# Optimization experiments

Hardware: AMD Instinct MI355X
Metric: run time of the kernel (lower is better)

## Reference

```python
import jax, jax.numpy as jnp
import numpy as np

B, T, S = 32, 64, 400
EMB = ENC = DEC = ATT = 512
POOL = 2
VOCAB = 32000
L = 1
NEG = 1e12  # INF constant from the torch source


def setup_inputs():
    key = jax.random.key(0)
    ks = jax.random.split(key, 16)
    def p(i, shape, s=0.05):
        return jax.random.normal(ks[i], shape, jnp.float32) * s
    return {
        "trg_seq_embedded": jax.random.normal(ks[0], (B, T, EMB), jnp.float32),
        "enc_states": jax.random.normal(ks[1], (L, B, ENC), jnp.float32),
        "encoder_outputs": jax.random.normal(ks[2], (B, S, ENC), jnp.float32),
        "W_trans": p(3, (DEC, ENC)), "b_trans": jnp.zeros((DEC,), jnp.float32),
        "W_ih": p(4, (3 * DEC, EMB + ENC)), "W_hh": p(5, (3 * DEC, DEC)),
        "b_ih": jnp.zeros((3 * DEC,), jnp.float32), "b_hh": jnp.zeros((3 * DEC,), jnp.float32),
        "W_pre": p(6, (ATT, ENC)), "b_pre": jnp.zeros((ATT,), jnp.float32),
        "W_q": p(7, (ATT, DEC)), "W_cov": p(8, (ATT, 1)), "v_att": p(9, (ATT,)),
        "W_ro": p(10, (DEC, ENC + DEC + EMB)), "b_ro": jnp.zeros((DEC,), jnp.float32),
        "W_logit": p(11, (VOCAB, DEC // POOL)), "b_logit": jnp.zeros((VOCAB,), jnp.float32),
        "ext_src_seq": jax.random.randint(ks[12], (B, S), 0, VOCAB + 50),
        "encoder_mask": jnp.zeros((B, S), jnp.bool_),  # True = padding position
    }


def _gru_cell(x, h, W_ih, W_hh, b_ih, b_hh):
    # torch.nn.GRUCell semantics, gate order r, z, n
    gi = x @ W_ih.T + b_ih
    gh = h @ W_hh.T + b_hh
    ir, iz, inn = jnp.split(gi, 3, axis=1)
    hr, hz, hn = jnp.split(gh, 3, axis=1)
    r = jax.nn.sigmoid(ir + hr)
    z = jax.nn.sigmoid(iz + hz)
    n = jnp.tanh(inn + r * hn)
    return (1.0 - z) * n + z * h


def _forward(trg, enc_states, memories, params, ext_src_seq, mask):
    (W_trans, b_trans, W_ih, W_hh, b_ih, b_hh, W_pre, b_pre, W_q, W_cov,
     v_att, W_ro, b_ro, W_logit, b_logit) = params
    # num_oov computed eagerly from the (constant) extended source ids
    num_oov = max(int(jnp.max(ext_src_seq)) - VOCAB + 1, 0)
    b_idx = jnp.arange(B)[:, None]
    precompute = memories @ W_pre.T + b_pre          # [B,S,ATT], computed once
    h0 = enc_states @ W_trans.T + b_trans            # [L,B,DEC] init_rnn_hidden
    c0 = jnp.zeros((B, ENC), trg.dtype)              # pre_context
    cov0 = jnp.zeros((B, S), trg.dtype)              # coverage

    def step(carry, emb):
        h, ctx, cov = carry
        x = jnp.concatenate([emb, ctx], axis=1)      # input_feed
        h_new = _gru_cell(x, h[0], W_ih, W_hh, b_ih, b_hh)  # single-layer StackedGRU
        out = h_new
        # ConcatAttention with coverage term
        target = out @ W_q.T                                    # [B,ATT]
        cov_term = cov[:, :, None] * W_cov[:, 0][None, None, :]  # [B,S,ATT]
        energy = jnp.tanh(precompute + target[:, None, :] + cov_term) @ v_att  # [B,S]
        energy = jnp.where(mask, -NEG, energy)
        score = jax.nn.softmax(energy, axis=1)
        context = jnp.einsum('bs,bse->be', score, memories)
        # readout -> maxout -> logits
        readout = jnp.concatenate([emb, out, context], axis=1) @ W_ro.T + b_ro
        mo = readout.reshape(B, DEC // POOL, POOL).max(axis=-1)
        logit = mo @ W_logit.T + b_logit
        # pointer: scatter_max of energy into extended vocab
        ext_logit = jnp.concatenate([logit, jnp.zeros((B, num_oov), logit.dtype)], axis=1)
        scat = jnp.full((B, VOCAB + num_oov), -NEG, logit.dtype)
        scat = scat.at[b_idx, ext_src_seq].max(energy)
        scat = jnp.where(scat == -NEG, 0.0, scat)
        logit = ext_logit + scat
        logit = jnp.where(logit == 0.0, -NEG, logit)
        return (h_new[None], context, cov + score), (logit, score, cov)

    _, (logits, attn, cov_hist) = jax.lax.scan(step, (h0, c0, cov0), jnp.swapaxes(trg, 0, 1))
    return jnp.swapaxes(logits, 0, 1), attn, cov_hist


def reference(trg_seq_embedded, enc_states, encoder_outputs, W_trans, b_trans, W_ih, W_hh, b_ih, b_hh, W_pre, b_pre, W_q, W_cov, v_att, W_ro, b_ro, W_logit, b_logit, ext_src_seq, encoder_mask):
    params = (W_trans, b_trans, W_ih, W_hh, b_ih, b_hh, W_pre, b_pre, W_q, W_cov,
              v_att, W_ro, b_ro, W_logit, b_logit)
    return _forward(trg_seq_embedded, enc_states, encoder_outputs, params, ext_src_seq, encoder_mask)
```

## Files before the change

kernel.cpp:

```cpp
#include <hip/hip_runtime.h>

#define Bz 32
#define Tz 64
#define Sz 400
#define Dz 512
#define G3 1536
#define VOC 32000
#define NEGC 1e12f
#define SB 50
#define JB 8

typedef __attribute__((ext_vector_type(8))) short short8;
typedef __attribute__((ext_vector_type(8))) _Float16 h8;
typedef __attribute__((ext_vector_type(4))) float f32x4;
typedef __attribute__((ext_vector_type(4))) unsigned u32x4;
typedef __attribute__((ext_vector_type(2))) _Float16 half2_t;

__device__ __forceinline__ float sigm(float x){ return 1.f/(1.f+__expf(-x)); }
__device__ __forceinline__ float tanhfast(float x){ float e=__expf(2.f*x); return 1.f - 2.f/(e+1.f); }
__device__ __forceinline__ unsigned short f2bf(float f){
  unsigned int u = __float_as_uint(f);
  u = (u + 0x7FFFu + ((u>>16)&1u)) >> 16;
  return (unsigned short)u;
}
__device__ __forceinline__ unsigned f2bf2(float a, float b){
  return (unsigned)f2bf(a) | ((unsigned)f2bf(b) << 16);
}
__device__ __forceinline__ half2_t bch2(unsigned u){ return __builtin_bit_cast(half2_t, u); }
__device__ __forceinline__ unsigned packh2(float a, float b){
  unsigned short ua = __builtin_bit_cast(unsigned short, (_Float16)a);
  unsigned short ub = __builtin_bit_cast(unsigned short, (_Float16)b);
  return (unsigned)ua | ((unsigned)ub << 16);
}

__device__ __forceinline__ float aload_f(const float* p){
  unsigned v = __hip_atomic_load((unsigned*)p, __ATOMIC_RELAXED, __HIP_MEMORY_SCOPE_AGENT);
  return __uint_as_float(v);
}
__device__ __forceinline__ unsigned long long aload_u64(const void* p){
  return __hip_atomic_load((const unsigned long long*)p, __ATOMIC_RELAXED, __HIP_MEMORY_SCOPE_AGENT);
}
__device__ __forceinline__ void astore_f(float* p, float v){
  __hip_atomic_store((unsigned*)p, __float_as_uint(v), __ATOMIC_RELAXED, __HIP_MEMORY_SCOPE_AGENT);
}
__device__ __forceinline__ void astore_u32(unsigned* p, unsigned v){
  __hip_atomic_store(p, v, __ATOMIC_RELAXED, __HIP_MEMORY_SCOPE_AGENT);
}

#if defined(__has_builtin)
#if __has_builtin(__builtin_amdgcn_fdot2)
#define HAVE_FDOT2 1
#endif
#endif
#ifdef HAVE_FDOT2
__device__ __forceinline__ float FDOT(half2_t a, half2_t b, float c){
  return __builtin_amdgcn_fdot2(a, b, c, false);
}
#else
__device__ __forceinline__ float FDOT(half2_t a, half2_t b, float c){
  return c + (float)a[0]*(float)b[0] + (float)a[1]*(float)b[1];
}
#endif

__global__ __launch_bounds__(128) void repack_emb(const float* __restrict__ emb,
    unsigned short* __restrict__ emb2, unsigned short* __restrict__ rinb){
  int tb = blockIdx.x; int t = tb >> 5, b = tb & 31;
  int e4 = threadIdx.x;
  float4 v = *(const float4*)&emb[((size_t)b*Tz + t)*Dz + e4*4];
  unsigned* e2 = (unsigned*)&emb2[(size_t)tb*Dz + e4*4];
  e2[0] = packh2(v.x, v.y);
  e2[1] = packh2(v.z, v.w);
  unsigned* rb = (unsigned*)&rinb[(size_t)tb*G3 + e4*4];
  rb[0] = f2bf2(v.x, v.y);
  rb[1] = f2bf2(v.z, v.w);
}

__global__ __launch_bounds__(256) void wgj_pack(const float* __restrict__ W_ih,
    const float* __restrict__ W_hh, unsigned* __restrict__ Wg){
  int idx = blockIdx.x*256 + threadIdx.x;
  int i = idx & 31, oct = (idx>>5)&7;
  int ks = idx >> 8;
  int s = ks % 6, k = ks / 6;
  int e0 = (oct*32 + i)*2;
  float w0, w1;
  if (s < 3){
    const float* base = W_ih + ((size_t)(s*512 + k))*1024 + 512;
    w0 = base[e0]; w1 = base[e0+1];
  } else {
    const float* base = W_hh + ((size_t)((s-3)*512 + k))*512;
    w0 = base[e0]; w1 = base[e0+1];
  }
  Wg[idx] = packh2(w0, w1);
}

__global__ __launch_bounds__(256) void wq2_pack(const float* __restrict__ W_q,
    unsigned* __restrict__ Wq2){
  int idx = blockIdx.x*256 + threadIdx.x;
  int jj = idx & 511;
  int i  = (idx>>9) & 31;
  int js = idx >> 14;
  int k0 = js*64 + 2*i;
  Wq2[idx] = packh2(W_q[(size_t)jj*512 + k0], W_q[(size_t)jj*512 + k0 + 1]);
}

__global__ __launch_bounds__(256) void cast_f16(const float* __restrict__ in,
    unsigned short* __restrict__ out, int n){
  for (int i = blockIdx.x*256 + threadIdx.x; i < n; i += gridDim.x*256)
    out[i] = __builtin_bit_cast(unsigned short, (_Float16)in[i]);
}

__global__ __launch_bounds__(256) void cast_f16_str(const float* __restrict__ in, int ldi,
    unsigned short* __restrict__ out, int cols, int n){
  for (int i = blockIdx.x*256 + threadIdx.x; i < n; i += gridDim.x*256){
    int r = i / cols, c = i - r*cols;
    out[i] = __builtin_bit_cast(unsigned short, (_Float16)in[(size_t)r*ldi + c]);
  }
}

__global__ __launch_bounds__(256) void cast_bf(const float* __restrict__ in,
    unsigned short* __restrict__ out, int n){
  for (int i = blockIdx.x*256 + threadIdx.x; i < n; i += gridDim.x*256)
    out[i] = f2bf(in[i]);
}

__global__ __launch_bounds__(256) void zero_u32(unsigned* __restrict__ p, int n){
  int i = blockIdx.x*256 + threadIdx.x;
  if (i < n) p[i] = 0u;
}

__global__ __launch_bounds__(256) void gemm_f32(const float* __restrict__ A, int lda,
    const float* __restrict__ Bm, int ldb, const float* __restrict__ bias,
    float* __restrict__ C, int ldc, int M, int N, int K){
  __shared__ __align__(16) float As[16][68];
  __shared__ __align__(16) float Bs[16][68];
  int tid = threadIdx.x;
  int m0 = blockIdx.x * 64, n0 = blockIdx.y * 64;
  int tx = tid & 15, ty = tid >> 4;
  float acc[4][4] = {};
  int lr = tid >> 2;
  int lk = (tid & 3) << 2;
  for (int k0 = 0; k0 < K; k0 += 16){
    int m = m0 + lr;
    float4 va = (m < M) ? *(const float4*)&A[(size_t)m*lda + k0 + lk] : make_float4(0,0,0,0);
    int n = n0 + lr;
    float4 vb = (n < N) ? *(const float4*)&Bm[(size_t)n*ldb + k0 + lk] : make_float4(0,0,0,0);
    As[lk+0][lr]=va.x; As[lk+1][lr]=va.y; As[lk+2][lr]=va.z; As[lk+3][lr]=va.w;
    Bs[lk+0][lr]=vb.x; Bs[lk+1][lr]=vb.y; Bs[lk+2][lr]=vb.z; Bs[lk+3][lr]=vb.w;
    __syncthreads();
    #pragma unroll
    for (int kk = 0; kk < 16; kk++){
      float4 a = *(const float4*)&As[kk][ty*4];
      float4 b = *(const float4*)&Bs[kk][tx*4];
      float av[4] = {a.x,a.y,a.z,a.w};
      float bv[4] = {b.x,b.y,b.z,b.w};
      #pragma unroll
      for (int i = 0; i < 4; i++)
        #pragma unroll
        for (int j = 0; j < 4; j++)
          acc[i][j] += av[i]*bv[j];
    }
    __syncthreads();
  }
  #pragma unroll
  for (int i = 0; i < 4; i++){
    int m = m0 + ty*4 + i;
    if (m >= M) continue;
    #pragma unroll
    for (int j = 0; j < 4; j++){
      int n = n0 + tx*4 + j;
      if (n < N) C[(size_t)m*ldc + n] = acc[i][j] + bias[n];
    }
  }
}

__global__ __launch_bounds__(256) void mfma_bf16(const unsigned short* __restrict__ A, int lda,
    const unsigned short* __restrict__ Bm, int ldb, const float* __restrict__ bias,
    float* __restrict__ out, int N, int K, int mode, int Vext){
  __shared__ __align__(16) unsigned short As[128][40];
  __shared__ __align__(16) unsigned short Bs[128][40];
  int tid = threadIdx.x;
  int m0 = blockIdx.x * 128, n0 = blockIdx.y * 128;
  int wid = tid >> 6, lane = tid & 63;
  int wm = (wid >> 1) * 64, wn = (wid & 1) * 64;
  f32x4 acc[4][4];
  #pragma unroll
  for (int r = 0; r < 4; r++)
    #pragma unroll
    for (int c = 0; c < 4; c++) acc[r][c] = (f32x4){0.f,0.f,0.f,0.f};
  int lr = tid >> 1;
  int lk = (tid & 1) * 16;
  int frow = lane & 15, kg = (lane >> 4) * 8;
  for (int k0 = 0; k0 < K; k0 += 32){
    *(uint4*)&As[lr][lk]     = *(const uint4*)&A[(size_t)(m0+lr)*lda + k0 + lk];
    *(uint4*)&As[lr][lk+8]   = *(const uint4*)&A[(size_t)(m0+lr)*lda + k0 + lk + 8];
    *(uint4*)&Bs[lr][lk]     = *(const uint4*)&Bm[(size_t)(n0+lr)*ldb + k0 + lk];
    *(uint4*)&Bs[lr][lk+8]   = *(const uint4*)&Bm[(size_t)(n0+lr)*ldb + k0 + lk + 8];
    __syncthreads();
    short8 af[4], bf[4];
    #pragma unroll
    for (int r = 0; r < 4; r++) af[r] = *(const short8*)&As[wm + r*16 + frow][kg];
    #pragma unroll
    for (int c = 0; c < 4; c++) bf[c] = *(const short8*)&Bs[wn + c*16 + frow][kg];
    #pragma unroll
    for (int r = 0; r < 4; r++)
      #pragma unroll
      for (int c = 0; c < 4; c++)
        acc[r][c] = __builtin_amdgcn_mfma_f32_16x16x32_bf16(af[r], bf[c], acc[r][c], 0, 0, 0);
    __syncthreads();
  }
  int crow = (lane >> 4) * 4, ccol = lane & 15;
  #pragma unroll
  for (int r = 0; r < 4; r++)
    #pragma unroll
    for (int c = 0; c < 4; c++)
      #pragma unroll
      for (int i = 0; i < 4; i++){
        int m = m0 + wm + r*16 + crow + i;
        int n = n0 + wn + c*16 + ccol;
        float v = acc[r][c][i] + bias[n];
        if (mode == 0){
          out[(size_t)m*N + n] = v;
        } else {
          int b = m & 31, t = m >> 5;
          v = (v == 0.f) ? -NEGC : v;
          out[((size_t)(b*Tz + t))*Vext + n] = v;
        }
      }
}

__global__ __launch_bounds__(256) void mfma_f16k(const unsigned short* __restrict__ A, int lda,
    const unsigned short* __restrict__ Bm, int ldb, const float* __restrict__ bias,
    void* __restrict__ outp, int N, int K, int mode){
  __shared__ __align__(16) unsigned short As[128][40];
  __shared__ __align__(16) unsigned short Bs[128][40];
  int tid = threadIdx.x;
  int m0 = blockIdx.x * 128, n0 = blockIdx.y * 128;
  int wid = tid >> 6, lane = tid & 63;
  int wm = (wid >> 1) * 64, wn = (wid & 1) * 64;
  f32x4 acc[4][4];
  #pragma unroll
  for (int r = 0; r < 4; r++)
    #pragma unroll
    for (int c = 0; c < 4; c++) acc[r][c] = (f32x4){0.f,0.f,0.f,0.f};
  int lr = tid >> 1;
  int lk = (tid & 1) * 16;
  int frow = lane & 15, kg = (lane >> 4) * 8;
  for (int k0 = 0; k0 < K; k0 += 32){
    *(uint4*)&As[lr][lk]     = *(const uint4*)&A[(size_t)(m0+lr)*lda + k0 + lk];
    *(uint4*)&As[lr][lk+8]   = *(const uint4*)&A[(size_t)(m0+lr)*lda + k0 + lk + 8];
    *(uint4*)&Bs[lr][lk]     = *(const uint4*)&Bm[(size_t)(n0+lr)*ldb + k0 + lk];
    *(uint4*)&Bs[lr][lk+8]   = *(const uint4*)&Bm[(size_t)(n0+lr)*ldb + k0 + lk + 8];
    __syncthreads();
    h8 af[4], bf[4];
    #pragma unroll
    for (int r = 0; r < 4; r++) af[r] = *(const h8*)&As[wm + r*16 + frow][kg];
    #pragma unroll
    for (int c = 0; c < 4; c++) bf[c] = *(const h8*)&Bs[wn + c*16 + frow][kg];
    #pragma unroll
    for (int r = 0; r < 4; r++)
      #pragma unroll
      for (int c = 0; c < 4; c++)
        acc[r][c] = __builtin_amdgcn_mfma_f32_16x16x32_f16(af[r], bf[c], acc[r][c], 0, 0, 0);
    __syncthreads();
  }
  int crow = (lane >> 4) * 4, ccol = lane & 15;
  #pragma unroll
  for (int r = 0; r < 4; r++)
    #pragma unroll
    for (int c = 0; c < 4; c++)
      #pragma unroll
      for (int i = 0; i < 4; i++){
        int m = m0 + wm + r*16 + crow + i;
        int n = n0 + wn + c*16 + ccol;
        float v = acc[r][c][i] + bias[n];
        if (mode == 0) ((float*)outp)[(size_t)m*N + n] = v;
        else ((unsigned short*)outp)[(size_t)m*N + n] =
               __builtin_bit_cast(unsigned short, (_Float16)v);
      }
}

struct PA {
  const unsigned* Wg; const unsigned* Wq2;
  const float* giE; const float* b_hh;
  const unsigned short* pre2; const unsigned short* mem2;
  const unsigned char* mask;
  const float* v_att; const float* w_cov;
  const float* hb;
  unsigned* hxG; unsigned* tgtG; unsigned* ctxG; float* denomG;
  unsigned* ctr;
  float* energyAll; unsigned short* rinb;
  float* attn_out; float* covh_out;
};

__device__ __forceinline__ void gbar(unsigned* ctr, unsigned target){
  __syncthreads();
  if (threadIdx.x == 0){
    __hip_atomic_fetch_add(ctr, 1u, __ATOMIC_RELEASE, __HIP_MEMORY_SCOPE_AGENT);
    unsigned v;
    do {
      v = __hip_atomic_load(ctr, __ATOMIC_RELAXED, __HIP_MEMORY_SCOPE_AGENT);
      if (v < target) __builtin_amdgcn_s_sleep(2);
    } while (v < target);
  }
  __syncthreads();
  asm volatile("" ::: "memory");
}

__global__ __launch_bounds__(512, 2) void step_all(PA P){
  const int bid = blockIdx.x, tid = threadIdx.x;
  const int b = bid >> 3, j = bid & 7;
  const int sbase = j * SB;
  const int wv = tid >> 6, l = tid & 63;

  __shared__ __align__(16) u32x4 pre_l4[SB*64];
  __shared__ __align__(16) u32x4 mem_l4[SB*64];
  __shared__ float ctxw[8*Dz];
  __shared__ float tgt_l[Dz];
  __shared__ __align__(16) unsigned c2p[8*36];
  __shared__ __align__(16) unsigned h2p[8*36];
  __shared__ unsigned hn2sl[32];
  __shared__ float hsl[64];
  __shared__ float gi6[192], bh6[192];
  __shared__ float covp[SB], pl[SB], wsum[8], sden[8];
  __shared__ unsigned char mk[SB];

  unsigned* ctr = P.ctr + b*16;
  unsigned barn = 0;

  f32x4 vva = *(const f32x4*)(P.v_att + l*8);
  f32x4 vvb = *(const f32x4*)(P.v_att + l*8 + 4);
  f32x4 wva = *(const f32x4*)(P.w_cov + l*8);
  f32x4 wvb = *(const f32x4*)(P.w_cov + l*8 + 4);

  const u32x4* WgJ4 = (const u32x4*)P.Wg;

  for (int t = 0; t < Tz; t++){
    if (t == 0){
      const u32x4* pq = (const u32x4*)P.pre2 + ((size_t)b*Sz + sbase)*64;
      const u32x4* mq = (const u32x4*)P.mem2 + ((size_t)b*Sz + sbase)*64;
      for (int v = tid; v < SB*64; v += 512){ pre_l4[v] = pq[v]; mem_l4[v] = mq[v]; }
      if (tid < 256){
        c2p[(tid>>5)*36 + (tid&31)] = 0u;
        float2 hv = *(const float2*)&P.hb[(size_t)b*Dz + 2*tid];
        h2p[(tid>>5)*36 + (tid&31)] = packh2(hv.x, hv.y);
      }
      if (tid < 64) hsl[tid] = P.hb[(size_t)b*Dz + j*64 + tid];
      if (tid >= 256 && tid < 256+SB){
        int s = tid - 256;
        covp[s] = 0.f;
        mk[s] = P.mask[b*Sz + sbase + s];
        P.covh_out[(size_t)b*Sz + sbase + s] = 0.f;
      }
      if (tid >= 320 && tid < 512){
        int idx = tid - 320;
        bh6[idx] = P.b_hh[(idx>>6)*512 + j*64 + (idx&63)];
        gi6[idx] = P.giE[(size_t)b*G3 + (idx>>6)*512 + j*64 + (idx&63)];
      }
    } else {
      barn++; gbar(ctr, JB*barn);
      if (tid < 8) sden[tid] = aload_f(&P.denomG[b*8 + tid]);
      __syncthreads();
      float invd = 1.f/(sden[0]+sden[1]+sden[2]+sden[3]+sden[4]+sden[5]+sden[6]+sden[7]);
      if (tid < 128){
        float c0=0.f, c1=0.f, c2=0.f, c3=0.f;
        #pragma unroll
        for (int jj = 0; jj < JB; jj++){
          unsigned long long v = aload_u64(&P.ctxG[((size_t)(b*8+jj))*256 + 2*tid]);
          float w = sden[jj];
          half2_t p0 = bch2((unsigned)v), p1 = bch2((unsigned)(v >> 32));
          c0 += w*(float)p0[0]; c1 += w*(float)p0[1];
          c2 += w*(float)p1[0]; c3 += w*(float)p1[1];
        }
        c0 *= invd; c1 *= invd; c2 *= invd; c3 *= invd;
        int p0i = 2*tid, p1i = 2*tid + 1;
        c2p[(p0i>>5)*36 + (p0i&31)] = packh2(c0, c1);
        c2p[(p1i>>5)*36 + (p1i&31)] = packh2(c2, c3);
        if ((tid >> 4) == j){
          unsigned* rp = (unsigned*)&P.rinb[((size_t)(t-1)*Bz + b)*G3 + 1024 + 4*tid];
          rp[0] = f2bf2(c0, c1); rp[1] = f2bf2(c2, c3);
        }
      } else if (tid >= 256 && tid < 256+SB){
        int s = tid - 256;
        float sp = pl[s]*invd;
        P.attn_out[((size_t)(t-1)*Bz + b)*Sz + sbase + s] = sp;
        float cc = covp[s] + sp;
        covp[s] = cc;
        P.covh_out[((size_t)t*Bz + b)*Sz + sbase + s] = cc;
      }
    }
    __syncthreads();

    {
      int k3 = tid >> 3, oct = tid & 7;
      float a0=0,a1=0,a2=0,a3=0,a4=0,a5=0;
      const u32x4* c4 = (const u32x4*)c2p + oct*9;
      const u32x4* h4 = (const u32x4*)h2p + oct*9;
      size_t wb = (((size_t)(j*64 + k3)*6)*8 + oct)*8;
      #pragma unroll 4
      for (int i = 0; i < 8; i++){
        u32x4 xc = c4[i];
        u32x4 xh = h4[i];
        u32x4 w0 = WgJ4[wb + i];
        u32x4 w1 = WgJ4[wb + 64 + i];
        u32x4 w2 = WgJ4[wb + 128 + i];
        u32x4 w3 = WgJ4[wb + 192 + i];
        u32x4 w4 = WgJ4[wb + 256 + i];
        u32x4 w5 = WgJ4[wb + 320 + i];
        #pragma unroll
        for (int q = 0; q < 4; q++){
          half2_t xcv = bch2(xc[q]), xhv = bch2(xh[q]);
          a0 = FDOT(bch2(w0[q]), xcv, a0);
          a1 = FDOT(bch2(w1[q]), xcv, a1);
          a2 = FDOT(bch2(w2[q]), xcv, a2);
          a3 = FDOT(bch2(w3[q]), xhv, a3);
          a4 = FDOT(bch2(w4[q]), xhv, a4);
          a5 = FDOT(bch2(w5[q]), xhv, a5);
        }
      }
      a0 += __shfl_xor(a0,1); a0 += __shfl_xor(a0,2); a0 += __shfl_xor(a0,4);
      a1 += __shfl_xor(a1,1); a1 += __shfl_xor(a1,2); a1 += __shfl_xor(a1,4);
      a2 += __shfl_xor(a2,1); a2 += __shfl_xor(a2,2); a2 += __shfl_xor(a2,4);
      a3 += __shfl_xor(a3,1); a3 += __shfl_xor(a3,2); a3 += __shfl_xor(a3,4);
      a4 += __shfl_xor(a4,1); a4 += __shfl_xor(a4,2); a4 += __shfl_xor(a4,4);
      a5 += __shfl_xor(a5,1); a5 += __shfl_xor(a5,2); a5 += __shfl_xor(a5,4);
      if (oct == 0){
        float gir = gi6[k3]     + a0;
        float giz = gi6[64+k3]  + a1;
        float gin = gi6[128+k3] + a2;
        float ghr = bh6[k3]     + a3;
        float ghz = bh6[64+k3]  + a4;
        float ghn = bh6[128+k3] + a5;
        float r = sigm(gir + ghr);
        float z = sigm(giz + ghz);
        float nn = tanhfast(gin + r*ghn);
        float hv = (1.f - z)*nn + z*hsl[k3];
        hsl[k3] = hv;
        P.rinb[((size_t)t*Bz + b)*G3 + 512 + j*64 + k3] = f2bf(hv);
      }
    }
    __syncthreads();
    if (tid < 32){
      unsigned hp = packh2(hsl[2*tid], hsl[2*tid+1]);
      hn2sl[tid] = hp;
      astore_u32(&P.hxG[b*256 + j*32 + tid], hp);
    }
    __syncthreads();
    {
      float f = 0.f;
      const unsigned* wq = P.Wq2 + (size_t)j*32*512 + tid;
      #pragma unroll 8
      for (int i = 0; i < 32; i++)
        f = FDOT(bch2(wq[(size_t)i*512]), bch2(hn2sl[i]), f);
      float fo = __shfl_xor(f, 1);
      if ((tid & 1) == 0)
        astore_u32(&P.tgtG[((size_t)(b*8+j))*256 + (tid>>1)], packh2(f, fo));
    }
    barn++; gbar(ctr, JB*barn);

    if (tid < 128){
      float t0=0.f, t1=0.f, t2=0.f, t3=0.f;
      #pragma unroll
      for (int jj = 0; jj < JB; jj++){
        unsigned long long v = aload_u64(&P.tgtG[((size_t)(b*8+jj))*256 + 2*tid]);
        half2_t p0 = bch2((unsigned)v), p1 = bch2((unsigned)(v >> 32));
        t0 += (float)p0[0]; t1 += (float)p0[1];
        t2 += (float)p1[0]; t3 += (float)p1[1];
      }
      tgt_l[4*tid] = t0; tgt_l[4*tid+1] = t1; tgt_l[4*tid+2] = t2; tgt_l[4*tid+3] = t3;
    } else if (tid < 256){
      int q = tid - 128;
      unsigned long long v = aload_u64(&P.hxG[b*256 + 2*q]);
      int p0i = 2*q, p1i = 2*q + 1;
      h2p[(p0i>>5)*36 + (p0i&31)] = (unsigned)v;
      h2p[(p1i>>5)*36 + (p1i&31)] = (unsigned)(v >> 32);
    }
    __syncthreads();
    {
      f32x4 t8a = *(const f32x4*)&tgt_l[l*8];
      f32x4 t8b = *(const f32x4*)&tgt_l[l*8 + 4];
      f32x4 ca = (f32x4){0.f,0.f,0.f,0.f}, cb = ca;
      float dsum = 0.f;
      #pragma unroll
      for (int i = 0; i < 7; i++){
        int s = wv + 8*i;
        if (s < SB){
          float cv = covp[s];
          int mkk = mk[s];
          u32x4 pq = pre_l4[s*64 + l];
          f32x4 ba = t8a + cv*wva, bb = t8b + cv*wvb;
          half2_t h0=bch2(pq[0]), h1=bch2(pq[1]), h2v=bch2(pq[2]), h3=bch2(pq[3]);
          float acc;
          acc  = vva[0]*tanhfast((float)h0[0] + ba[0]);
          acc += vva[1]*tanhfast((float)h0[1] + ba[1]);
          acc += vva[2]*tanhfast((float)h1[0] + ba[2]);
          acc += vva[3]*tanhfast((float)h1[1] + ba[3]);
          acc += vvb[0]*tanhfast((float)h2v[0] + bb[0]);
          acc += vvb[1]*tanhfast((float)h2v[1] + bb[1]);
          acc += vvb[2]*tanhfast((float)h3[0] + bb[2]);
          acc += vvb[3]*tanhfast((float)h3[1] + bb[3]);
          #pragma unroll
          for (int m = 1; m < 64; m <<= 1) acc += __shfl_xor(acc, m);
          float en = mkk ? -NEGC : acc;
          float p = __expf(en);
          if (l == 0){
            P.energyAll[((size_t)t*Bz + b)*Sz + sbase + s] = en;
            pl[s] = p;
            dsum += p;
          }
          u32x4 mq = mem_l4[s*64 + l];
          half2_t m0=bch2(mq[0]), m1=bch2(mq[1]), m2=bch2(mq[2]), m3=bch2(mq[3]);
          ca[0] += p*(float)m0[0]; ca[1] += p*(float)m0[1];
          ca[2] += p*(float)m1[0]; ca[3] += p*(float)m1[1];
          cb[0] += p*(float)m2[0]; cb[1] += p*(float)m2[1];
          cb[2] += p*(float)m3[0]; cb[3] += p*(float)m3[1];
        }
      }
      if (l == 0) wsum[wv] = dsum;
      *(f32x4*)&ctxw[wv*Dz + l*8]     = ca;
      *(f32x4*)&ctxw[wv*Dz + l*8 + 4] = cb;
    }
    __syncthreads();
    {
      float ds = wsum[0]+wsum[1]+wsum[2]+wsum[3]+wsum[4]+wsum[5]+wsum[6]+wsum[7];
      float rden = (ds > 0.f) ? 1.f/ds : 0.f;
      float cs = 0.f;
      #pragma unroll
      for (int w = 0; w < 8; w++) cs += ctxw[w*Dz + tid];
      cs *= rden;
      float co = __shfl_xor(cs, 1);
      if ((tid & 1) == 0)
        astore_u32(&P.ctxG[((size_t)(b*8+j))*256 + (tid>>1)], packh2(cs, co));
      if (tid == 0) astore_f(&P.denomG[b*8 + j], ds);
    }
    if (t+1 < Tz && tid >= 320){
      int idx = tid - 320;
      gi6[idx] = P.giE[((size_t)(t+1)*Bz + b)*G3 + (idx>>6)*512 + j*64 + (idx&63)];
    }
  }

  barn++; gbar(ctr, JB*barn);
  {
    if (tid < 8) sden[tid] = aload_f(&P.denomG[b*8 + tid]);
    __syncthreads();
    float invd = 1.f/(sden[0]+sden[1]+sden[2]+sden[3]+sden[4]+sden[5]+sden[6]+sden[7]);
    if (tid < 128 && (tid >> 4) == j){
      float c0=0.f, c1=0.f, c2=0.f, c3=0.f;
      #pragma unroll
      for (int jj = 0; jj < JB; jj++){
        unsigned long long v = aload_u64(&P.ctxG[((size_t)(b*8+jj))*256 + 2*tid]);
        float w = sden[jj];
        half2_t p0 = bch2((unsigned)v), p1 = bch2((unsigned)(v >> 32));
        c0 += w*(float)p0[0]; c1 += w*(float)p0[1];
        c2 += w*(float)p1[0]; c3 += w*(float)p1[1];
      }
      unsigned* rp = (unsigned*)&P.rinb[((size_t)63*Bz + b)*G3 + 1024 + 4*tid];
      rp[0] = f2bf2(c0*invd, c1*invd); rp[1] = f2bf2(c2*invd, c3*invd);
    } else if (tid >= 256 && tid < 256+SB){
      int s = tid - 256;
      P.attn_out[((size_t)63*Bz + b)*Sz + sbase + s] = pl[s]*invd;
    }
  }
}

__global__ __launch_bounds__(256) void maxout_k(const float* __restrict__ rout,
    unsigned short* __restrict__ mo){
  int m = blockIdx.x, d = threadIdx.x;
  float a = rout[(size_t)m*Dz + 2*d], b = rout[(size_t)m*Dz + 2*d + 1];
  mo[(size_t)m*256 + d] = f2bf(fmaxf(a, b));
}

__global__ __launch_bounds__(64) void oov_fill(float* __restrict__ out, int Vext){
  int m = blockIdx.x;
  int b = m & 31, t = m >> 5;
  size_t base = (size_t)(b*Tz + t) * Vext;
  for (int v = VOC + threadIdx.x; v < Vext; v += 64)
    out[base + v] = -NEGC;
}

__global__ __launch_bounds__(256) void scatter_k(const int* __restrict__ ext,
    const float* __restrict__ energyAll, float* __restrict__ out, int Vext){
  __shared__ int ex[Sz];
  __shared__ float en[Sz];
  int m = blockIdx.x;
  int t = m >> 5, b = m & 31;
  int tid = threadIdx.x;
  for (int s = tid; s < Sz; s += 256){
    ex[s] = ext[b*Sz + s];
    en[s] = energyAll[(size_t)m*Sz + s];
  }
  __syncthreads();
  size_t base = (size_t)(b*Tz + t) * Vext;
  for (int s = tid; s < Sz; s += 256){
    int v = ex[s];
    float mv = -3.4e38f; int idx = -1;
    for (int s2 = 0; s2 < Sz; s2++){
      if (ex[s2] == v && en[s2] > mv){ mv = en[s2]; idx = s2; }
    }
    if (idx == s && mv != -NEGC){
      if (v < VOC){
        float w = out[base + v] + mv;
        out[base + v] = (w == 0.f) ? -NEGC : w;
      } else {
        out[base + v] = (mv == 0.f) ? -NEGC : mv;
      }
    }
  }
}

extern "C" void kernel_launch(void* const* d_in, const int* in_sizes, int n_in,
                              void* d_out, int out_size, void* d_ws, size_t ws_size,
                              hipStream_t stream){
  const float* emb     = (const float*)d_in[0];
  const float* enc0    = (const float*)d_in[1];
  const float* mem     = (const float*)d_in[2];
  const float* W_trans = (const float*)d_in[3];
  const float* b_trans = (const float*)d_in[4];
  const float* W_ih    = (const float*)d_in[5];
  const float* W_hh    = (const float*)d_in[6];
  const float* b_ih    = (const float*)d_in[7];
  const float* b_hh    = (const float*)d_in[8];
  const float* W_pre   = (const float*)d_in[9];
  const float* b_pre   = (const float*)d_in[10];
  const float* W_q     = (const float*)d_in[11];
  const float* W_cov   = (const float*)d_in[12];
  const float* v_att   = (const float*)d_in[13];
  const float* W_ro    = (const float*)d_in[14];
  const float* b_ro    = (const float*)d_in[15];
  const float* W_logit = (const float*)d_in[16];
  const float* b_logit = (const float*)d_in[17];
  const int*   ext     = (const int*)d_in[18];
  const unsigned char* maskp = (const unsigned char*)d_in[19];
  float* out = (float*)d_out;

  const int Vext = (out_size - 2*Tz*Bz*Sz) / (Bz*Tz);

  char* ws = (char*)d_ws;
  size_t off = 0;
  auto alloc = [&](size_t bytes)->void*{
    void* p = ws + off;
    off += (bytes + 255) & ~(size_t)255;
    return p;
  };
  float* giE         = (float*)alloc((size_t)Tz*Bz*G3*4);
  unsigned* Wg       = (unsigned*)alloc((size_t)786432*4);
  unsigned* Wq2      = (unsigned*)alloc((size_t)131072*4);
  unsigned short* pre2 = (unsigned short*)alloc((size_t)Bz*Sz*Dz*2);
  unsigned short* mem2 = (unsigned short*)alloc((size_t)Bz*Sz*Dz*2);
  unsigned short* emb2 = (unsigned short*)alloc((size_t)Tz*Bz*Dz*2);
  unsigned short* Wih2 = (unsigned short*)alloc((size_t)G3*Dz*2);
  unsigned short* Wpre2= (unsigned short*)alloc((size_t)Dz*Dz*2);
  float* hb          = (float*)alloc((size_t)Bz*Dz*4);
  unsigned* hxG      = (unsigned*)alloc((size_t)Bz*256*4);
  unsigned* tgtG     = (unsigned*)alloc((size_t)Bz*JB*256*4);
  unsigned* ctxG     = (unsigned*)alloc((size_t)Bz*JB*256*4);
  float* denomG      = (float*)alloc((size_t)Bz*JB*4);
  unsigned* ctr      = (unsigned*)alloc((size_t)Bz*16*4);
  float* energyAll   = (float*)alloc((size_t)Tz*Bz*Sz*4);
  float* rout        = (float*)alloc((size_t)Tz*Bz*Dz*4);
  unsigned short* rin_bf = (unsigned short*)alloc((size_t)Tz*Bz*G3*2);
  unsigned short* Wro_bf = (unsigned short*)alloc((size_t)Dz*G3*2);
  unsigned short* mo_bf  = (unsigned short*)alloc((size_t)Tz*Bz*256*2);
  unsigned short* Wl_bf  = (unsigned short*)alloc((size_t)VOC*256*2);

  float* attn_out = out + (size_t)Bz*Tz*Vext;
  float* covh_out = attn_out + (size_t)Tz*Bz*Sz;

  repack_emb<<<Tz*Bz, 128, 0, stream>>>(emb, emb2, rin_bf);
  wgj_pack<<<3072, 256, 0, stream>>>(W_ih, W_hh, Wg);
  wq2_pack<<<512, 256, 0, stream>>>(W_q, Wq2);
  zero_u32<<<2, 256, 0, stream>>>(ctr, Bz*16);
  cast_f16<<<2048, 256, 0, stream>>>(mem, mem2, Bz*Sz*Dz);
  cast_f16_str<<<1024, 256, 0, stream>>>(W_ih, 1024, Wih2, 512, G3*Dz);
  cast_f16<<<512, 256, 0, stream>>>(W_pre, (unsigned short*)Wpre2, Dz*Dz);
  gemm_f32<<<dim3(1, Dz/64), 256, 0, stream>>>(enc0, Dz, W_trans, Dz, b_trans, hb, Dz, Bz, Dz, Dz);
  mfma_f16k<<<dim3(Tz*Bz/128, G3/128), 256, 0, stream>>>(emb2, Dz, Wih2, Dz, b_ih,
                                                         giE, G3, Dz, 0);
  mfma_f16k<<<dim3(Bz*Sz/128, Dz/128), 256, 0, stream>>>(mem2, Dz, Wpre2, Dz, b_pre,
                                                         pre2, Dz, Dz, 2);
  cast_bf<<<1024, 256, 0, stream>>>(W_ro, Wro_bf, Dz*G3);
  cast_bf<<<2048, 256, 0, stream>>>(W_logit, Wl_bf, VOC*256);

  PA P;
  P.Wg = Wg; P.Wq2 = Wq2; P.giE = giE; P.b_hh = b_hh;
  P.pre2 = pre2; P.mem2 = mem2; P.mask = maskp; P.v_att = v_att; P.w_cov = W_cov;
  P.hb = hb; P.hxG = hxG; P.tgtG = tgtG; P.ctxG = ctxG; P.denomG = denomG;
  P.ctr = ctr; P.energyAll = energyAll; P.rinb = rin_bf;
  P.attn_out = attn_out; P.covh_out = covh_out;
  void* kargs[] = { (void*)&P };
  hipLaunchCooperativeKernel((void*)step_all, dim3(Bz*JB), dim3(512), kargs, 0, stream);

  mfma_bf16<<<dim3(Tz*Bz/128, Dz/128), 256, 0, stream>>>(rin_bf, G3, Wro_bf, G3, b_ro,
                                                         rout, Dz, G3, 0, 0);
  maxout_k<<<Tz*Bz, 256, 0, stream>>>(rout, mo_bf);
  mfma_bf16<<<dim3(Tz*Bz/128, VOC/128), 256, 0, stream>>>(mo_bf, 256, Wl_bf, 256, b_logit,
                                                          out, VOC, 256, 1, Vext);
  oov_fill<<<Tz*Bz, 64, 0, stream>>>(out, Vext);
  scatter_k<<<Tz*Bz, 256, 0, stream>>>(ext, energyAll, out, Vext);
  (void)in_sizes; (void)n_in; (void)ws_size;
}
```

Measured before the change: 2.132 ms.

## Assign blocks to batch groups by XCC so grid barriers stay within one die

Each block reads its XCC id from a hardware register and claims a (batch, slice) slot through atomic counters, so the 8 blocks sharing a batch's grid barrier land on the same XCC where possible. When a batch group is fully co-located, cross-block exchanges use plain volatile loads and stores instead of agent-scope atomics. The aim is to cut cross-die coherence latency in the per-step barriers and data exchange. The cost is an extra startup barrier and claim logic. Using volatile accesses instead of agent-scope atomics depends on the same-XCC L2 being coherent, which is a correctness risk if that assumption is wrong.

Result: slower. 2.343 ms (+9.9%).

```diff
diff --git a/kernel.cpp b/kernel.cpp
--- a/kernel.cpp
+++ b/kernel.cpp
@@ -40,11 +40,27 @@
 __device__ __forceinline__ unsigned long long aload_u64(const void* p){
   return __hip_atomic_load((const unsigned long long*)p, __ATOMIC_RELAXED, __HIP_MEMORY_SCOPE_AGENT);
 }
+__device__ __forceinline__ int aload_i(const unsigned* p){
+  return (int)__hip_atomic_load(p, __ATOMIC_RELAXED, __HIP_MEMORY_SCOPE_AGENT);
+}
 __device__ __forceinline__ void astore_f(float* p, float v){
   __hip_atomic_store((unsigned*)p, __float_as_uint(v), __ATOMIC_RELAXED, __HIP_MEMORY_SCOPE_AGENT);
 }
 __device__ __forceinline__ void astore_u32(unsigned* p, unsigned v){
   __hip_atomic_store(p, v, __ATOMIC_RELAXED, __HIP_MEMORY_SCOPE_AGENT);
+}
+
+__device__ __forceinline__ unsigned long long xload_u64(const void* p, bool pure){
+  return pure ? *(volatile const unsigned long long*)p : aload_u64(p);
+}
+__device__ __forceinline__ float xload_f(const float* p, bool pure){
+  return pure ? *(volatile const float*)p : aload_f(p);
+}
+__device__ __forceinline__ void xstore_u32(unsigned* p, unsigned v, bool pure){
+  if (pure) *(volatile unsigned*)p = v; else astore_u32(p, v);
+}
+__device__ __forceinline__ void xstore_f(float* p, float v, bool pure){
+  if (pure) *(volatile float*)p = v; else astore_f(p, v);
 }
 
 #if defined(__has_builtin)
@@ -307,9 +323,7 @@
 }
 
 __global__ __launch_bounds__(512, 2) void step_all(PA P){
-  const int bid = blockIdx.x, tid = threadIdx.x;
-  const int b = bid >> 3, j = bid & 7;
-  const int sbase = j * SB;
+  const int tid = threadIdx.x;
   const int wv = tid >> 6, l = tid & 63;
 
   __shared__ __align__(16) u32x4 pre_l4[SB*64];
@@ -323,8 +337,43 @@
   __shared__ float gi6[192], bh6[192];
   __shared__ float covp[SB], pl[SB], wsum[8], sden[8];
   __shared__ unsigned char mk[SB];
-
-  unsigned* ctr = P.ctr + b*16;
+  __shared__ int sjb[4];
+
+  unsigned* claim = P.ctr + Bz*32;
+  if (tid == 0){
+    unsigned xcc = __builtin_amdgcn_s_getreg((31u<<11) | 20u) & 7u;
+    unsigned r = __hip_atomic_fetch_add(&claim[xcc], 1u, __ATOMIC_RELAXED, __HIP_MEMORY_SCOPE_AGENT);
+    sjb[0] = (int)xcc; sjb[1] = (int)r;
+  }
+  gbar(&claim[12], 256);
+  if (tid == 0){
+    int xcc = sjb[0], r = sjb[1];
+    int bb, jj;
+    if (r < 32){ bb = xcc*4 + (r>>3); jj = r & 7; }
+    else {
+      int o = (int)__hip_atomic_fetch_add(&claim[8], 1u, __ATOMIC_RELAXED, __HIP_MEMORY_SCOPE_AGENT);
+      bb = 31; jj = 7;
+      int cnt = 0;
+      for (int k = 0; k < 8; k++){
+        int used = aload_i(&claim[k]);
+        if (used > 32) used = 32;
+        int fr = 32 - used;
+        if (o >= cnt && o < cnt + fr){
+          int rr = used + (o - cnt);
+          bb = k*4 + (rr>>3); jj = rr & 7;
+        }
+        cnt += fr;
+      }
+    }
+    int X = bb >> 2, g = bb & 3;
+    int cx = aload_i(&claim[X]);
+    sjb[0] = bb; sjb[1] = jj; sjb[2] = (cx >= 8*(g+1)) ? 1 : 0;
+  }
+  __syncthreads();
+  const int b = sjb[0], j = sjb[1];
+  const bool pure = (sjb[2] != 0);
+  const int sbase = j * SB;
+  unsigned* ctr = P.ctr + b*32;
   unsigned barn = 0;
 
   f32x4 vva = *(const f32x4*)(P.v_att + l*8);
@@ -358,14 +407,14 @@
       }
     } else {
       barn++; gbar(ctr, JB*barn);
-      if (tid < 8) sden[tid] = aload_f(&P.denomG[b*8 + tid]);
+      if (tid < 8) sden[tid] = xload_f(&P.denomG[b*8 + tid], pure);
       __syncthreads();
       float invd = 1.f/(sden[0]+sden[1]+sden[2]+sden[3]+sden[4]+sden[5]+sden[6]+sden[7]);
       if (tid < 128){
         float c0=0.f, c1=0.f, c2=0.f, c3=0.f;
         #pragma unroll
         for (int jj = 0; jj < JB; jj++){
-          unsigned long long v = aload_u64(&P.ctxG[((size_t)(b*8+jj))*256 + 2*tid]);
+          unsigned long long v = xload_u64(&P.ctxG[((size_t)(b*8+jj))*256 + 2*tid], pure);
           float w = sden[jj];
           half2_t p0 = bch2((unsigned)v), p1 = bch2((unsigned)(v >> 32));
           c0 += w*(float)p0[0]; c1 += w*(float)p0[1];
@@ -442,7 +491,7 @@
     if (tid < 32){
       unsigned hp = packh2(hsl[2*tid], hsl[2*tid+1]);
       hn2sl[tid] = hp;
-      astore_u32(&P.hxG[b*256 + j*32 + tid], hp);
+      xstore_u32(&P.hxG[b*256 + j*32 + tid], hp, pure);
     }
     __syncthreads();
     {
@@ -453,7 +502,7 @@
         f = FDOT(bch2(wq[(size_t)i*512]), bch2(hn2sl[i]), f);
       float fo = __shfl_xor(f, 1);
       if ((tid & 1) == 0)
-        astore_u32(&P.tgtG[((size_t)(b*8+j))*256 + (tid>>1)], packh2(f, fo));
+        xstore_u32(&P.tgtG[((size_t)(b*8+j))*256 + (tid>>1)], packh2(f, fo), pure);
     }
     barn++; gbar(ctr, JB*barn);
 
@@ -461,7 +510,7 @@
       float t0=0.f, t1=0.f, t2=0.f, t3=0.f;
       #pragma unroll
       for (int jj = 0; jj < JB; jj++){
-        unsigned long long v = aload_u64(&P.tgtG[((size_t)(b*8+jj))*256 + 2*tid]);
+        unsigned long long v = xload_u64(&P.tgtG[((size_t)(b*8+jj))*256 + 2*tid], pure);
         half2_t p0 = bch2((unsigned)v), p1 = bch2((unsigned)(v >> 32));
         t0 += (float)p0[0]; t1 += (float)p0[1];
         t2 += (float)p1[0]; t3 += (float)p1[1];
@@ -469,7 +518,7 @@
       tgt_l[4*tid] = t0; tgt_l[4*tid+1] = t1; tgt_l[4*tid+2] = t2; tgt_l[4*tid+3] = t3;
     } else if (tid < 256){
       int q = tid - 128;
-      unsigned long long v = aload_u64(&P.hxG[b*256 + 2*q]);
+      unsigned long long v = xload_u64(&P.hxG[b*256 + 2*q], pure);
       int p0i = 2*q, p1i = 2*q + 1;
       h2p[(p0i>>5)*36 + (p0i&31)] = (unsigned)v;
       h2p[(p1i>>5)*36 + (p1i&31)] = (unsigned)(v >> 32);
@@ -529,8 +578,8 @@
       cs *= rden;
       float co = __shfl_xor(cs, 1);
       if ((tid & 1) == 0)
-        astore_u32(&P.ctxG[((size_t)(b*8+j))*256 + (tid>>1)], packh2(cs, co));
-      if (tid == 0) astore_f(&P.denomG[b*8 + j], ds);
+        xstore_u32(&P.ctxG[((size_t)(b*8+j))*256 + (tid>>1)], packh2(cs, co), pure);
+      if (tid == 0) xstore_f(&P.denomG[b*8 + j], ds, pure);
     }
     if (t+1 < Tz && tid >= 320){
       int idx = tid - 320;
@@ -540,14 +589,14 @@
 
   barn++; gbar(ctr, JB*barn);
   {
-    if (tid < 8) sden[tid] = aload_f(&P.denomG[b*8 + tid]);
+    if (tid < 8) sden[tid] = xload_f(&P.denomG[b*8 + tid], pure);
     __syncthreads();
     float invd = 1.f/(sden[0]+sden[1]+sden[2]+sden[3]+sden[4]+sden[5]+sden[6]+sden[7]);
     if (tid < 128 && (tid >> 4) == j){
       float c0=0.f, c1=0.f, c2=0.f, c3=0.f;
       #pragma unroll
       for (int jj = 0; jj < JB; jj++){
-        unsigned long long v = aload_u64(&P.ctxG[((size_t)(b*8+jj))*256 + 2*tid]);
+        unsigned long long v = xload_u64(&P.ctxG[((size_t)(b*8+jj))*256 + 2*tid], pure);
         float w = sden[jj];
         half2_t p0 = bch2((unsigned)v), p1 = bch2((unsigned)(v >> 32));
         c0 += w*(float)p0[0]; c1 += w*(float)p0[1];
@@ -654,7 +703,7 @@
   unsigned* tgtG     = (unsigned*)alloc((size_t)Bz*JB*256*4);
   unsigned* ctxG     = (unsigned*)alloc((size_t)Bz*JB*256*4);
   float* denomG      = (float*)alloc((size_t)Bz*JB*4);
-  unsigned* ctr      = (unsigned*)alloc((size_t)Bz*16*4);
+  unsigned* ctr      = (unsigned*)alloc((size_t)(Bz*32 + 16)*4);
   float* energyAll   = (float*)alloc((size_t)Tz*Bz*Sz*4);
   float* rout        = (float*)alloc((size_t)Tz*Bz*Dz*4);
   unsigned short* rin_bf = (unsigned short*)alloc((size_t)Tz*Bz*G3*2);
@@ -668,7 +717,7 @@
   repack_emb<<<Tz*Bz, 128, 0, stream>>>(emb, emb2, rin_bf);
   wgj_pack<<<3072, 256, 0, stream>>>(W_ih, W_hh, Wg);
   wq2_pack<<<512, 256, 0, stream>>>(W_q, Wq2);
-  zero_u32<<<2, 256, 0, stream>>>(ctr, Bz*16);
+  zero_u32<<<5, 256, 0, stream>>>(ctr, Bz*32 + 16);
   cast_f16<<<2048, 256, 0, stream>>>(mem, mem2, Bz*Sz*Dz);
   cast_f16_str<<<1024, 256, 0, stream>>>(W_ih, 1024, Wih2, 512, G3*Dz);
   cast_f16<<<512, 256, 0, stream>>>(W_pre, (unsigned short*)Wpre2, Dz*Dz);
```
